# Kernel tuning notes

Measured on AMD Instinct MI355X. Metric: run time of the kernel, lower is better.

## Reference

```python
import jax, jax.numpy as jnp
import numpy as np


def _normalize(x):
    # channel mean-subtract then channel L2 normalize, as in MIDMs.forward
    x = x - x.mean(axis=1, keepdims=True)
    return x / jnp.linalg.norm(x, axis=1, keepdims=True)


def setup_inputs() -> dict:
    key = jax.random.key(0)
    ks = jax.random.split(key, 6)
    B, C, H, W = 2, 256, 64, 64
    return {
        "trg_out": jax.random.normal(ks[0], (B, C, H, W), jnp.float32),
        "src_out": jax.random.normal(ks[1], (B, C, H, W), jnp.float32),
        "ref_out": jax.random.normal(ks[2], (B, C, H, W), jnp.float32),
        "src_feats": jax.random.normal(ks[3], (B, 4, H, W), jnp.float32),
        "ref_feats": jax.random.normal(ks[4], (B, 4, H, W), jnp.float32),
        "ref_semantics": jax.random.uniform(ks[5], (B, 151, H, W), jnp.float32),
    }


def reference(trg_out, src_out, ref_out, src_feats, ref_feats, ref_semantics):
    B, C, H, W = trg_out.shape
    L = H * W
    # normalized matching features, flattened over spatial positions
    t = _normalize(trg_out).reshape(B, C, L)   # [B, C, Lt]
    s = _normalize(src_out).reshape(B, C, L)   # [B, C, Ls]
    r = _normalize(ref_out).reshape(B, C, L)

    # Correlation.correlation: dense cosine affinity between all position pairs
    corr_src = jnp.einsum("bci,bcj->bij", t, s)  # [B, Lt, Ls]
    corr_ref = jnp.einsum("bci,bcj->bij", t, r)

    # soft_warp: softmax over source positions, attention-weighted gather
    attn_src = jax.nn.softmax(corr_src, axis=-1)
    attn_ref = jax.nn.softmax(corr_ref, axis=-1)

    warped_src_feat = jnp.einsum("bij,bcj->bci", attn_src,
                                 src_feats.reshape(B, -1, L)).reshape(B, -1, H, W)
    warped_ref_feat = jnp.einsum("bij,bcj->bci", attn_ref,
                                 ref_feats.reshape(B, -1, L)).reshape(B, -1, H, W)
    warped_ref_seg = jnp.einsum("bij,bcj->bci", attn_ref,
                                ref_semantics.reshape(B, -1, L)).reshape(B, -1, H, W)
    return warped_src_feat, warped_ref_feat, warped_ref_seg
```

## Files before the change

kernel.cpp:

```cpp
#include <hip/hip_runtime.h>
#include <hip/hip_bf16.h>
#include <cstdint>
#include <cstddef>

typedef unsigned short u16;
typedef __attribute__((ext_vector_type(8))) __bf16 bf16x8;
typedef __attribute__((ext_vector_type(4))) unsigned u32x4;
typedef __attribute__((ext_vector_type(16))) float f32x16;

#define LPOS 4096
#define CDIM 256
#define LDSBUF 13312

#if __has_builtin(__builtin_amdgcn_exp2f)
#define EXP2(x) __builtin_amdgcn_exp2f(x)
#else
#define EXP2(x) exp2f(x)
#endif

#define GLOAD_LDS16(g, l)                                                      \
  __builtin_amdgcn_global_load_lds(                                            \
      (const __attribute__((address_space(1))) void*)(g),                      \
      (__attribute__((address_space(3))) void*)(l), 16, 0, 0)

__device__ __forceinline__ unsigned f2bfbits(float x) {
  union { float f; unsigned u; } v; v.f = x;
  return (v.u + 0x7FFFu + ((v.u >> 16) & 1u)) >> 16;
}
__device__ __forceinline__ unsigned packbf(float a, float b) {
  __hip_bfloat162 h2 = __float22bfloat162_rn(make_float2(a, b));
  return *(unsigned*)&h2;
}

__global__ void norm_fused(const float* __restrict__ t_in,
                           const float* __restrict__ s_in,
                           const float* __restrict__ r_in,
                           u16* __restrict__ qn, u16* __restrict__ ksn,
                           u16* __restrict__ krn) {
  __shared__ float tile[256 * 33];
  __shared__ float sums[256], sqs[256];
  __shared__ float mv[32], ivv[32];
  int idx = blockIdx.x;
  int ab = idx >> 7, lt = idx & 127;
  int arr = ab >> 1, b = ab & 1;
  int l0 = lt * 32;
  const float* inp = (arr == 0 ? t_in : arr == 1 ? s_in : r_in) + (size_t)b * CDIM * LPOS;
  u16* outp = (arr == 0 ? qn : arr == 1 ? ksn : krn) + (size_t)b * LPOS * CDIM;
  float scale = (arr == 0) ? 1.4426950408889634f : 1.0f;
  int t = threadIdx.x;
  int cg = t >> 5, l = t & 31;
  float sum = 0.f, sq = 0.f;
#pragma unroll 8
  for (int cc = 0; cc < 32; ++cc) {
    int c = cg * 32 + cc;
    float v = inp[(size_t)c * LPOS + l0 + l];
    tile[c * 33 + l] = v;
    sum += v; sq += v * v;
  }
  sums[t] = sum; sqs[t] = sq;
  __syncthreads();
  if (t < 32) {
    float s = 0.f, q = 0.f;
#pragma unroll
    for (int g = 0; g < 8; ++g) { s += sums[g * 32 + t]; q += sqs[g * 32 + t]; }
    float mean = s * (1.0f / CDIM);
    float nsq = q - s * s * (1.0f / CDIM);
    mv[t] = mean;
    ivv[t] = rsqrtf(fmaxf(nsq, 1e-20f)) * scale;
  }
  __syncthreads();
  int c2 = t & 127, ph = t >> 7;
#pragma unroll 4
  for (int rr = 0; rr < 16; ++rr) {
    int pos = ph + rr * 2;
    float m = mv[pos], iv = ivv[pos];
    float v0 = (tile[(2 * c2) * 33 + pos] - m) * iv;
    float v1 = (tile[(2 * c2 + 1) * 33 + pos] - m) * iv;
    *(unsigned*)&outp[(size_t)(l0 + pos) * CDIM + 2 * c2] = packbf(v0, v1);
  }
}

__global__ void build_v(const float* __restrict__ sf, const float* __restrict__ rf,
                        const float* __restrict__ sem,
                        u16* __restrict__ vs, u16* __restrict__ vr) {
  int t = blockIdx.x * 256 + threadIdx.x;
  const int NVS = 2 * 32 * 4096;
  if (t < NVS) {
    int b = t >> 17;
    int c = (t >> 12) & 31;
    int j = t & 4095;
    float v = (c < 4) ? sf[((size_t)b * 4 + c) * LPOS + j] : (c == 4 ? 1.0f : 0.0f);
    vs[t] = (u16)f2bfbits(v);
  } else {
    int t2 = t - NVS;
    if (t2 < 2 * 160 * 4096) {
      int b = t2 / (160 * 4096);
      int rr = t2 % (160 * 4096);
      int c = rr >> 12, j = rr & 4095;
      float v = (c < 151) ? sem[((size_t)b * 151 + c) * LPOS + j]
              : (c < 155) ? rf[((size_t)b * 4 + (c - 151)) * LPOS + j]
              : (c == 155) ? 1.0f : 0.0f;
      vr[((size_t)b * 160 + c) * LPOS + j] = (u16)f2bfbits(v);
    }
  }
}

template <int CT>
__device__ __forceinline__ void flash_body(
    const u16* __restrict__ qb, const u16* __restrict__ kb,
    const u16* __restrict__ vb, float* __restrict__ dst,
    u16 (*lds)[LDSBUF], int wave, int lane, int i_wave, int j_base, int iters) {
  int h = lane >> 5, ln = lane & 31;

  bf16x8 qf[16];
  const u16* qrow = qb + (size_t)(i_wave + ln) * CDIM;
#pragma unroll
  for (int kt = 0; kt < 16; ++kt)
    qf[kt] = *(const bf16x8*)(qrow + kt * 16 + h * 8);
#pragma unroll
  for (int kt = 0; kt < 16; ++kt)
    asm volatile("" : "+v"(*(u32x4*)&qf[kt]));

  f32x16 O[CT];
#pragma unroll
  for (int c = 0; c < CT; ++c)
#pragma unroll
    for (int t = 0; t < 16; ++t) O[c][t] = 0.0f;

  auto stage = [&](int j0s, int buf) {
#pragma unroll
    for (int g = 0; g < 2; ++g) {
      int G = wave * 2 + g;
      int j = 2 * G + h;
      GLOAD_LDS16(kb + (size_t)(j0s + j) * CDIM + (ln ^ (j & 7)) * 8,
                  &lds[buf][G * 512]);
    }
    if constexpr (CT == 5) {
#pragma unroll
      for (int g = 0; g < 2; ++g) {
        int s = wave + g * 8;
        if (s < 10) {
          int f = s * 64 + lane;
          int p = f / 160;
          int c = f - p * 160;
          GLOAD_LDS16(vb + (size_t)c * LPOS + j0s + p * 8,
                      &lds[buf][8192 + s * 512]);
        }
      }
    }
  };

  int kread_base = ln * 256 + 8 * (h ^ (ln & 1));
  int q = (ln >> 1) & 3;
  const u16* ka[4];
#pragma unroll
  for (int m = 0; m < 4; ++m) ka[m] = &lds[0][kread_base + 16 * (m ^ q)];
  const u16* va = &lds[0][8192 + h * 1280 + ln * 8];

  f32x16 Sp;
#pragma unroll
  for (int t = 0; t < 16; ++t) Sp[t] = 0.0f;

  auto finish_prev = [&](int pbo, const bf16x8* vfp) {
    f32x16 S;
#pragma unroll
    for (int t = 0; t < 16; ++t) S[t] = EXP2(Sp[t]);
    bf16x8 pb[2];
#pragma unroll
    for (int kh = 0; kh < 2; ++kh) {
      unsigned c0 = packbf(S[kh * 8 + 0], S[kh * 8 + 1]);
      unsigned c1 = packbf(S[kh * 8 + 2], S[kh * 8 + 3]);
      unsigned c2 = packbf(S[kh * 8 + 4], S[kh * 8 + 5]);
      unsigned c3 = packbf(S[kh * 8 + 6], S[kh * 8 + 7]);
      asm("v_permlane32_swap_b32 %0, %1" : "+v"(c0), "+v"(c2));
      asm("v_permlane32_swap_b32 %0, %1" : "+v"(c1), "+v"(c3));
      union { unsigned u[4]; bf16x8 v; } tmp;
      tmp.u[0] = c0;
      tmp.u[1] = c1;
      tmp.u[2] = c2;
      tmp.u[3] = c3;
      pb[kh] = tmp.v;
    }
#pragma unroll
    for (int ct = 0; ct < CT; ++ct)
#pragma unroll
      for (int kt2 = 0; kt2 < 2; ++kt2) {
        bf16x8 vax;
        if constexpr (CT == 5)
          vax = *(const bf16x8*)(va + kt2 * 2560 + ct * 256 + pbo);
        else
          vax = vfp[kt2];
        O[ct] = __builtin_amdgcn_mfma_f32_32x32x16_bf16(vax, pb[kt2], O[ct], 0, 0, 0);
      }
  };

  stage(j_base, 0);

  int buf = 0, pbo = 0;
  for (int jt = 0; jt < iters; ++jt) {
    int j0 = j_base + jt * 32;
    int bo = buf * LDSBUF;

    asm volatile("s_waitcnt vmcnt(0)" ::: "memory");
    __builtin_amdgcn_sched_barrier(0);
    __builtin_amdgcn_s_barrier();
    __builtin_amdgcn_sched_barrier(0);

    bf16x8 vf[2];
    if (CT == 1 && jt >= 1) {
#pragma unroll
      for (int kt2 = 0; kt2 < 2; ++kt2)
        vf[kt2] = *(const bf16x8*)(vb + (size_t)ln * LPOS + (j0 - 32) + (2 * kt2 + h) * 8);
    }
    if (jt + 1 < iters) {
      int nb = (buf == 2) ? 0 : buf + 1;
      stage(j0 + 32, nb);
    }

    __builtin_amdgcn_s_setprio(1);

    f32x16 Sa, Sb;
#pragma unroll
    for (int t = 0; t < 16; ++t) { Sa[t] = 0.0f; Sb[t] = 0.0f; }
#pragma unroll
    for (int kt = 0; kt < 16; kt += 2) {
      bf16x8 ka0 = *(const bf16x8*)(ka[kt & 3] + 64 * (kt >> 2) + bo);
      Sa = __builtin_amdgcn_mfma_f32_32x32x16_bf16(ka0, qf[kt], Sa, 0, 0, 0);
      bf16x8 ka1 = *(const bf16x8*)(ka[(kt + 1) & 3] + 64 * ((kt + 1) >> 2) + bo);
      Sb = __builtin_amdgcn_mfma_f32_32x32x16_bf16(ka1, qf[kt + 1], Sb, 0, 0, 0);
    }

    if (jt >= 1) finish_prev(pbo, vf);

#pragma unroll
    for (int t = 0; t < 16; ++t) Sp[t] = Sa[t] + Sb[t];

    __builtin_amdgcn_s_setprio(0);

    pbo = bo;
    buf = (buf == 2) ? 0 : buf + 1;
  }

  {
    bf16x8 vf[2];
    if constexpr (CT == 1) {
      int jlast = j_base + (iters - 1) * 32;
#pragma unroll
      for (int kt2 = 0; kt2 < 2; ++kt2)
        vf[kt2] = *(const bf16x8*)(vb + (size_t)ln * LPOS + jlast + (2 * kt2 + h) * 8);
    }
    finish_prev(pbo, vf);
  }

  const int climit = (CT == 1) ? 5 : 156;
#pragma unroll
  for (int ct = 0; ct < CT; ++ct)
#pragma unroll
    for (int t = 0; t < 16; ++t) {
      int c = ct * 32 + (t & 3) + 8 * (t >> 2) + 4 * h;
      if (c < climit)
        dst[(size_t)c * LPOS + i_wave + ln] = O[ct][t];
    }
}

__global__ __launch_bounds__(512, 2) void flash(
    const u16* __restrict__ qn, const u16* __restrict__ ksn, const u16* __restrict__ krn,
    const u16* __restrict__ vs, const u16* __restrict__ vr,
    float* __restrict__ nsrc, float* __restrict__ nref,
    int nch_src, int nch_ref) {
  __shared__ u16 lds[3][LDSBUF];
  int tid = threadIdx.x;
  int wave = tid >> 6, lane = tid & 63;
  int idx = blockIdx.x;
  int nrefb = 32 * nch_ref;
  int wsub = (wave & 3) * 32 + (wave >> 2) * 128;
  if (idx < nrefb) {
    int r = idx;
    int chunk = r >> 5, b = (r >> 4) & 1, wgi = r & 15;
    int jchunk = LPOS / nch_ref;
    flash_body<5>(qn + (size_t)b * LPOS * CDIM, krn + (size_t)b * LPOS * CDIM,
                  vr + (size_t)b * 160 * LPOS,
                  nref + (size_t)(chunk * 2 + b) * 160 * LPOS,
                  lds, wave, lane, wgi * 256 + wsub, chunk * jchunk,
                  jchunk / 32);
  } else {
    int r = idx - nrefb;
    int chunk = r >> 5, b = (r >> 4) & 1, wgi = r & 15;
    int jchunk = LPOS / nch_src;
    flash_body<1>(qn + (size_t)b * LPOS * CDIM, ksn + (size_t)b * LPOS * CDIM,
                  vs + (size_t)b * 32 * LPOS,
                  nsrc + (size_t)(chunk * 2 + b) * 32 * LPOS,
                  lds, wave, lane, wgi * 256 + wsub, chunk * jchunk,
                  jchunk / 32);
  }
}

__global__ void finalize(const float* __restrict__ nsrc, const float* __restrict__ nref,
                         float* __restrict__ out, int nch_src, int nch_ref) {
  int v = blockIdx.x * 256 + threadIdx.x;
  if (v >= 325632) return;
  float nx = 0.f, ny = 0.f, nz = 0.f, nw = 0.f;
  float dx = 0.f, dy = 0.f, dz = 0.f, dw = 0.f;
  if (v < 8192) {
    int b = v >> 12, c = (v >> 10) & 3, i4 = v & 1023;
    for (int k = 0; k < nch_src; ++k) {
      const float* base = nsrc + ((size_t)(k * 2 + b) * 32) * LPOS;
      float4 n4 = ((const float4*)(base + (size_t)c * LPOS))[i4];
      float4 d4 = ((const float4*)(base + (size_t)4 * LPOS))[i4];
      nx += n4.x; ny += n4.y; nz += n4.z; nw += n4.w;
      dx += d4.x; dy += d4.y; dz += d4.z; dw += d4.w;
    }
  } else if (v < 16384) {
    int v1 = v - 8192;
    int b = v1 >> 12, c = (v1 >> 10) & 3, i4 = v1 & 1023;
    for (int k = 0; k < nch_ref; ++k) {
      const float* base = nref + ((size_t)(k * 2 + b) * 160) * LPOS;
      float4 n4 = ((const float4*)(base + (size_t)(151 + c) * LPOS))[i4];
      float4 d4 = ((const float4*)(base + (size_t)155 * LPOS))[i4];
      nx += n4.x; ny += n4.y; nz += n4.z; nw += n4.w;
      dx += d4.x; dy += d4.y; dz += d4.z; dw += d4.w;
    }
  } else {
    int v2 = v - 16384;
    int b = v2 / 154624;
    int rr = v2 - b * 154624;
    int c = rr >> 10, i4 = rr & 1023;
    for (int k = 0; k < nch_ref; ++k) {
      const float* base = nref + ((size_t)(k * 2 + b) * 160) * LPOS;
      float4 n4 = ((const float4*)(base + (size_t)c * LPOS))[i4];
      float4 d4 = ((const float4*)(base + (size_t)155 * LPOS))[i4];
      nx += n4.x; ny += n4.y; nz += n4.z; nw += n4.w;
      dx += d4.x; dy += d4.y; dz += d4.z; dw += d4.w;
    }
  }
  float4 r;
  r.x = nx / dx; r.y = ny / dy; r.z = nz / dz; r.w = nw / dw;
  ((float4*)out)[v] = r;
}

extern "C" void kernel_launch(void* const* d_in, const int* in_sizes, int n_in,
                              void* d_out, int out_size, void* d_ws, size_t ws_size,
                              hipStream_t stream) {
  const float* trg  = (const float*)d_in[0];
  const float* srcp = (const float*)d_in[1];
  const float* refp = (const float*)d_in[2];
  const float* sfeat = (const float*)d_in[3];
  const float* rfeat = (const float*)d_in[4];
  const float* rsem  = (const float*)d_in[5];
  float* out = (float*)d_out;

  char* ws = (char*)d_ws;
  size_t o = 0;
  auto alloc = [&](size_t bytes) -> char* {
    char* p = ws + o;
    o += (bytes + 255) & ~(size_t)255;
    return p;
  };
  u16* qn  = (u16*)alloc(2ull * LPOS * CDIM * 2);
  u16* ksn = (u16*)alloc(2ull * LPOS * CDIM * 2);
  u16* krn = (u16*)alloc(2ull * LPOS * CDIM * 2);
  u16* vs  = (u16*)alloc(2ull * 32 * LPOS * 2);
  u16* vr  = (u16*)alloc(2ull * 160 * LPOS * 2);

  size_t fixed = o;
  int nch_ref = 8;
  for (;;) {
    size_t need = fixed + 512 +
                  (size_t)nch_ref * 2 * 32 * LPOS * 4 +
                  (size_t)nch_ref * 2 * 160 * LPOS * 4;
    if (need <= ws_size || nch_ref == 1) break;
    nch_ref >>= 1;
  }
  int nch_src = nch_ref;
  float* nsrc = (float*)alloc((size_t)nch_src * 2 * 32 * LPOS * 4);
  float* nref = (float*)alloc((size_t)nch_ref * 2 * 160 * LPOS * 4);

  hipLaunchKernelGGL(norm_fused, dim3(768), dim3(256), 0, stream,
                     trg, srcp, refp, qn, ksn, krn);
  hipLaunchKernelGGL(build_v, dim3(6144), dim3(256), 0, stream,
                     sfeat, rfeat, rsem, vs, vr);
  hipLaunchKernelGGL(flash, dim3(32 * (nch_ref + nch_src)), dim3(512), 0, stream,
                     qn, ksn, krn, vs, vr, nsrc, nref, nch_src, nch_ref);
  hipLaunchKernelGGL(finalize, dim3(1272), dim3(256), 0, stream,
                     nsrc, nref, out, nch_src, nch_ref);
}
```

Measured before the change: 147.7 us.

## Accumulate split-K flash partials with float atomics instead of per-chunk buffers

Each split-K chunk of the flash kernel now atomically adds its unnormalized numerator and denominator into a single shared accumulator, instead of writing to a private per-chunk slice. The accumulator is zeroed inside build_v, and finalize reads one value per element rather than summing over chunks. This removes the large partial-buffer writes and the multi-chunk reduction reads, at the cost of atomic contention from 8 chunks hitting the same addresses. Float summation order also becomes nondeterministic.

```diff
diff --git a/kernel.cpp b/kernel.cpp
--- a/kernel.cpp
+++ b/kernel.cpp
@@ -11,6 +11,8 @@
 #define LPOS 4096
 #define CDIM 256
 #define LDSBUF 13312
+#define RACC_N (2 * 156 * LPOS)
+#define SACC_N (2 * 5 * LPOS)
 
 #if __has_builtin(__builtin_amdgcn_exp2f)
 #define EXP2(x) __builtin_amdgcn_exp2f(x)
@@ -82,8 +84,10 @@
 
 __global__ void build_v(const float* __restrict__ sf, const float* __restrict__ rf,
                         const float* __restrict__ sem,
-                        u16* __restrict__ vs, u16* __restrict__ vr) {
+                        u16* __restrict__ vs, u16* __restrict__ vr,
+                        float* __restrict__ zacc) {
   int t = blockIdx.x * 256 + threadIdx.x;
+  if (t < RACC_N + SACC_N) zacc[t] = 0.0f;
   const int NVS = 2 * 32 * 4096;
   if (t < NVS) {
     int b = t >> 17;
@@ -259,14 +263,14 @@
     for (int t = 0; t < 16; ++t) {
       int c = ct * 32 + (t & 3) + 8 * (t >> 2) + 4 * h;
       if (c < climit)
-        dst[(size_t)c * LPOS + i_wave + ln] = O[ct][t];
+        atomicAdd(&dst[(size_t)c * LPOS + i_wave + ln], O[ct][t]);
     }
 }
 
 __global__ __launch_bounds__(512, 2) void flash(
     const u16* __restrict__ qn, const u16* __restrict__ ksn, const u16* __restrict__ krn,
     const u16* __restrict__ vs, const u16* __restrict__ vr,
-    float* __restrict__ nsrc, float* __restrict__ nref,
+    float* __restrict__ sacc, float* __restrict__ racc,
     int nch_src, int nch_ref) {
   __shared__ u16 lds[3][LDSBUF];
   int tid = threadIdx.x;
@@ -280,7 +284,7 @@
     int jchunk = LPOS / nch_ref;
     flash_body<5>(qn + (size_t)b * LPOS * CDIM, krn + (size_t)b * LPOS * CDIM,
                   vr + (size_t)b * 160 * LPOS,
-                  nref + (size_t)(chunk * 2 + b) * 160 * LPOS,
+                  racc + (size_t)b * 156 * LPOS,
                   lds, wave, lane, wgi * 256 + wsub, chunk * jchunk,
                   jchunk / 32);
   } else {
@@ -289,52 +293,39 @@
     int jchunk = LPOS / nch_src;
     flash_body<1>(qn + (size_t)b * LPOS * CDIM, ksn + (size_t)b * LPOS * CDIM,
                   vs + (size_t)b * 32 * LPOS,
-                  nsrc + (size_t)(chunk * 2 + b) * 32 * LPOS,
+                  sacc + (size_t)b * 5 * LPOS,
                   lds, wave, lane, wgi * 256 + wsub, chunk * jchunk,
                   jchunk / 32);
   }
 }
 
-__global__ void finalize(const float* __restrict__ nsrc, const float* __restrict__ nref,
-                         float* __restrict__ out, int nch_src, int nch_ref) {
+__global__ void finalize(const float* __restrict__ sacc, const float* __restrict__ racc,
+                         float* __restrict__ out) {
   int v = blockIdx.x * 256 + threadIdx.x;
   if (v >= 325632) return;
-  float nx = 0.f, ny = 0.f, nz = 0.f, nw = 0.f;
-  float dx = 0.f, dy = 0.f, dz = 0.f, dw = 0.f;
+  float4 n4, d4;
   if (v < 8192) {
     int b = v >> 12, c = (v >> 10) & 3, i4 = v & 1023;
-    for (int k = 0; k < nch_src; ++k) {
-      const float* base = nsrc + ((size_t)(k * 2 + b) * 32) * LPOS;
-      float4 n4 = ((const float4*)(base + (size_t)c * LPOS))[i4];
-      float4 d4 = ((const float4*)(base + (size_t)4 * LPOS))[i4];
-      nx += n4.x; ny += n4.y; nz += n4.z; nw += n4.w;
-      dx += d4.x; dy += d4.y; dz += d4.z; dw += d4.w;
-    }
+    const float* base = sacc + (size_t)b * 5 * LPOS;
+    n4 = ((const float4*)(base + (size_t)c * LPOS))[i4];
+    d4 = ((const float4*)(base + (size_t)4 * LPOS))[i4];
   } else if (v < 16384) {
     int v1 = v - 8192;
     int b = v1 >> 12, c = (v1 >> 10) & 3, i4 = v1 & 1023;
-    for (int k = 0; k < nch_ref; ++k) {
-      const float* base = nref + ((size_t)(k * 2 + b) * 160) * LPOS;
-      float4 n4 = ((const float4*)(base + (size_t)(151 + c) * LPOS))[i4];
-      float4 d4 = ((const float4*)(base + (size_t)155 * LPOS))[i4];
-      nx += n4.x; ny += n4.y; nz += n4.z; nw += n4.w;
-      dx += d4.x; dy += d4.y; dz += d4.z; dw += d4.w;
-    }
+    const float* base = racc + (size_t)b * 156 * LPOS;
+    n4 = ((const float4*)(base + (size_t)(151 + c) * LPOS))[i4];
+    d4 = ((const float4*)(base + (size_t)155 * LPOS))[i4];
   } else {
     int v2 = v - 16384;
     int b = v2 / 154624;
     int rr = v2 - b * 154624;
     int c = rr >> 10, i4 = rr & 1023;
-    for (int k = 0; k < nch_ref; ++k) {
-      const float* base = nref + ((size_t)(k * 2 + b) * 160) * LPOS;
-      float4 n4 = ((const float4*)(base + (size_t)c * LPOS))[i4];
-      float4 d4 = ((const float4*)(base + (size_t)155 * LPOS))[i4];
-      nx += n4.x; ny += n4.y; nz += n4.z; nw += n4.w;
-      dx += d4.x; dy += d4.y; dz += d4.z; dw += d4.w;
-    }
+    const float* base = racc + (size_t)b * 156 * LPOS;
+    n4 = ((const float4*)(base + (size_t)c * LPOS))[i4];
+    d4 = ((const float4*)(base + (size_t)155 * LPOS))[i4];
   }
   float4 r;
-  r.x = nx / dx; r.y = ny / dy; r.z = nz / dz; r.w = nw / dw;
+  r.x = n4.x / d4.x; r.y = n4.y / d4.y; r.z = n4.z / d4.z; r.w = n4.w / d4.w;
   ((float4*)out)[v] = r;
 }
 
@@ -361,26 +352,18 @@
   u16* krn = (u16*)alloc(2ull * LPOS * CDIM * 2);
   u16* vs  = (u16*)alloc(2ull * 32 * LPOS * 2);
   u16* vr  = (u16*)alloc(2ull * 160 * LPOS * 2);
-
-  size_t fixed = o;
+  float* racc = (float*)alloc((size_t)(RACC_N + SACC_N) * 4);
+  float* sacc = racc + RACC_N;
+
   int nch_ref = 8;
-  for (;;) {
-    size_t need = fixed + 512 +
-                  (size_t)nch_ref * 2 * 32 * LPOS * 4 +
-                  (size_t)nch_ref * 2 * 160 * LPOS * 4;
-    if (need <= ws_size || nch_ref == 1) break;
-    nch_ref >>= 1;
-  }
-  int nch_src = nch_ref;
-  float* nsrc = (float*)alloc((size_t)nch_src * 2 * 32 * LPOS * 4);
-  float* nref = (float*)alloc((size_t)nch_ref * 2 * 160 * LPOS * 4);
+  int nch_src = 8;
 
   hipLaunchKernelGGL(norm_fused, dim3(768), dim3(256), 0, stream,
                      trg, srcp, refp, qn, ksn, krn);
   hipLaunchKernelGGL(build_v, dim3(6144), dim3(256), 0, stream,
-                     sfeat, rfeat, rsem, vs, vr);
+                     sfeat, rfeat, rsem, vs, vr, racc);
   hipLaunchKernelGGL(flash, dim3(32 * (nch_ref + nch_src)), dim3(512), 0, stream,
-                     qn, ksn, krn, vs, vr, nsrc, nref, nch_src, nch_ref);
+                     qn, ksn, krn, vs, vr, sacc, racc, nch_src, nch_ref);
   hipLaunchKernelGGL(finalize, dim3(1272), dim3(256), 0, stream,
-                     nsrc, nref, out, nch_src, nch_ref);
-}
+                     sacc, racc, out);
+}
```

Result: slower. 172.5 us (+16.8%).
